# Kernel tuning notes

Measured on AMD Instinct MI355X. Metric: run time of the kernel, lower is better.

The kernel has to match this reference:

```python
import jax, jax.numpy as jnp
import numpy as np

EPS = 1e-8  # torch F.cosine_similarity denominator clamp
NEG = -1e9

def setup_inputs() -> dict:
    key = jax.random.key(0)
    k1, k2, k3 = jax.random.split(key, 3)
    B, H, L, D = 16, 16, 4096, 128
    query = jax.random.normal(k1, (B, H, 1, D), dtype=jnp.float32)
    key_t = jax.random.normal(k2, (B, H, L, D), dtype=jnp.float32)
    mask = jax.random.randint(k3, (B, L), 0, 2, dtype=jnp.int32)
    return {"query": query, "key": key_t, "mask": mask}

def reference(query, key, mask):
    # cosine similarity without materializing the repeated query:
    # scores[b,h,l] = <q[b,h,0],k[b,h,l]> / max(||q||*||k||, eps)
    dots = jnp.einsum('bhod,bhld->bhl', query, key)  # o == 1, [B,H,L]
    qn = jnp.linalg.norm(query, axis=3)              # [B,H,1]
    kn = jnp.linalg.norm(key, axis=3)                # [B,H,L]
    scores = dots / jnp.maximum(qn * kn, EPS)        # [B,H,L]
    m = mask[:, None, :]                              # [B,1,L] broadcast over H
    scores = jnp.where(m == 0, NEG, scores)
    p_attn = jax.nn.softmax(scores, axis=2)
    return p_attn
```

## Files before the change

kernel.cpp:

```cpp
#include <hip/hip_runtime.h>
#include <hip/hip_bf16.h>


constexpr int Bdim = 16, Hdim = 16, Ldim = 4096, Ddim = 128;
constexpr int NTHREADS = 1024;
constexpr float EPSF = 1e-8f;
constexpr float NEGF = -1000000000.0f;

__device__ __forceinline__ float dpp_sum32(float v) {
    v += __int_as_float(__builtin_amdgcn_update_dpp(0, __float_as_int(v), 0x111, 0xf, 0xf, true));
    v += __int_as_float(__builtin_amdgcn_update_dpp(0, __float_as_int(v), 0x112, 0xf, 0xf, true));
    v += __int_as_float(__builtin_amdgcn_update_dpp(0, __float_as_int(v), 0x114, 0xf, 0xf, true));
    v += __int_as_float(__builtin_amdgcn_update_dpp(0, __float_as_int(v), 0x118, 0xf, 0xf, true));
    v += __int_as_float(__builtin_amdgcn_update_dpp(0, __float_as_int(v), 0x142, 0xa, 0xf, true));
    return v;
}

__global__ __launch_bounds__(NTHREADS, 1) void attn_cos_softmax(
    const float* __restrict__ q,
    const float* __restrict__ k,
    const int* __restrict__ mask,
    float* __restrict__ out)
{
    const int bh = blockIdx.x;
    const int b  = bh >> 4;
    const float4* qrow = reinterpret_cast<const float4*>(q + (size_t)bh * Ddim);
    const float4* krow = reinterpret_cast<const float4*>(k + (size_t)bh * Ldim * Ddim);
    const int*    mrow = mask + (size_t)b * Ldim;
    float*        orow = out  + (size_t)bh * Ldim;

    __shared__ float s_scores[Ldim];
    __shared__ float s_redmax[16];
    __shared__ float s_redsum[16];

    const int tid  = threadIdx.x;
    const int g    = tid >> 5;
    const int lane = tid & 31;
    const bool writer = (lane == 31);

    float4 qv = qrow[lane];
    float q2 = qv.x*qv.x + qv.y*qv.y + qv.z*qv.z + qv.w*qv.w;
    q2 = dpp_sum32(q2);
    const float qn = sqrtf(q2);

    constexpr int UNROLL = 16;
    constexpr int ROWS_PER_ITER = 32 * UNROLL;
    #pragma unroll 1
    for (int iter = 0; iter < Ldim / ROWS_PER_ITER; ++iter) {
        const int base = iter * ROWS_PER_ITER + g;
        float4 kv[UNROLL];
        #pragma unroll
        for (int j = 0; j < UNROLL; ++j) {
            kv[j] = krow[(base + j * 32) * (Ddim / 4) + lane];
        }
        #pragma unroll
        for (int j = 0; j < UNROLL; ++j) {
            float dp = kv[j].x*qv.x + kv[j].y*qv.y + kv[j].z*qv.z + kv[j].w*qv.w;
            float k2 = kv[j].x*kv[j].x + kv[j].y*kv[j].y + kv[j].z*kv[j].z + kv[j].w*kv[j].w;
            dp = dpp_sum32(dp);
            k2 = dpp_sum32(k2);
            if (writer) {
                float denom = fmaxf(qn * sqrtf(k2), EPSF);
                s_scores[base + j * 32] = dp / denom;
            }
        }
    }
    __syncthreads();

    float sv[4];
    float lmax = -3.0e9f;
    #pragma unroll
    for (int i = 0; i < 4; ++i) {
        const int idx = tid + i * NTHREADS;
        float s = s_scores[idx];
        s = (mrow[idx] == 0) ? NEGF : s;
        sv[i] = s;
        lmax = fmaxf(lmax, s);
    }
    #pragma unroll
    for (int m = 32; m >= 1; m >>= 1) lmax = fmaxf(lmax, __shfl_xor(lmax, m));
    if ((tid & 63) == 0) s_redmax[tid >> 6] = lmax;
    __syncthreads();
    float gmax = s_redmax[0];
    #pragma unroll
    for (int i = 1; i < 16; ++i) gmax = fmaxf(gmax, s_redmax[i]);

    float ev[4];
    float lsum = 0.0f;
    #pragma unroll
    for (int i = 0; i < 4; ++i) {
        ev[i] = __expf(sv[i] - gmax);
        lsum += ev[i];
    }
    #pragma unroll
    for (int m = 32; m >= 1; m >>= 1) lsum += __shfl_xor(lsum, m);
    if ((tid & 63) == 0) s_redsum[tid >> 6] = lsum;
    __syncthreads();
    float gsum = 0.0f;
    #pragma unroll
    for (int i = 0; i < 16; ++i) gsum += s_redsum[i];
    const float rinv = 1.0f / gsum;

    #pragma unroll
    for (int i = 0; i < 4; ++i) {
        orow[tid + i * NTHREADS] = ev[i] * rinv;
    }
}

extern "C" void kernel_launch(void* const* d_in, const int* in_sizes, int n_in,
                              void* d_out, int out_size, void* d_ws, size_t ws_size,
                              hipStream_t stream) {
    const float* q    = (const float*)d_in[0];
    const float* k    = (const float*)d_in[1];
    const int*   mask = (const int*)d_in[2];
    float*       out  = (float*)d_out;

    dim3 grid(Bdim * Hdim);
    dim3 block(NTHREADS);
    attn_cos_softmax<<<grid, block, 0, stream>>>(q, k, mask, out);
}
```

Before: 104.4 us.

## Split into chunked score kernel and separate vectorized softmax kernel

Splits the fused per-(b,h) kernel into two launches. The first computes cosine scores with 8 chunks per head and 256-thread blocks, raising occupancy to better hide the latency of streaming the keys. The second applies the mask and softmax with float4/int4 vector loads. Scores now round-trip through global memory in the output buffer, and the second launch adds its own overhead.

```diff
diff --git a/kernel.cpp b/kernel.cpp
--- a/kernel.cpp
+++ b/kernel.cpp
@@ -3,7 +3,6 @@
 
 
 constexpr int Bdim = 16, Hdim = 16, Ldim = 4096, Ddim = 128;
-constexpr int NTHREADS = 1024;
 constexpr float EPSF = 1e-8f;
 constexpr float NEGF = -1000000000.0f;
 
@@ -16,22 +15,26 @@
     return v;
 }
 
-__global__ __launch_bounds__(NTHREADS, 1) void attn_cos_softmax(
+constexpr int K1_THREADS = 256;
+constexpr int K1_CHUNKS  = 8;
+constexpr int K1_ROWS    = Ldim / K1_CHUNKS;
+constexpr int K1_UNROLL  = 4;
+constexpr int K1_GROUPS  = K1_THREADS / 32;
+constexpr int K1_RPI     = K1_GROUPS * K1_UNROLL;
+
+__global__ __launch_bounds__(K1_THREADS, 8) void attn_scores(
     const float* __restrict__ q,
     const float* __restrict__ k,
-    const int* __restrict__ mask,
-    float* __restrict__ out)
+    float* __restrict__ scores)
 {
-    const int bh = blockIdx.x;
-    const int b  = bh >> 4;
-    const float4* qrow = reinterpret_cast<const float4*>(q + (size_t)bh * Ddim);
-    const float4* krow = reinterpret_cast<const float4*>(k + (size_t)bh * Ldim * Ddim);
-    const int*    mrow = mask + (size_t)b * Ldim;
-    float*        orow = out  + (size_t)bh * Ldim;
+    const int bid   = blockIdx.x;
+    const int bh    = bid >> 3;
+    const int chunk = bid & (K1_CHUNKS - 1);
+    const int rowbase = chunk * K1_ROWS;
 
-    __shared__ float s_scores[Ldim];
-    __shared__ float s_redmax[16];
-    __shared__ float s_redsum[16];
+    const float4* qrow  = reinterpret_cast<const float4*>(q + (size_t)bh * Ddim);
+    const float4* krow  = reinterpret_cast<const float4*>(k + (size_t)bh * Ldim * Ddim);
+    float*        srow  = scores + (size_t)bh * Ldim;
 
     const int tid  = threadIdx.x;
     const int g    = tid >> 5;
@@ -43,67 +46,84 @@
     q2 = dpp_sum32(q2);
     const float qn = sqrtf(q2);
 
-    constexpr int UNROLL = 16;
-    constexpr int ROWS_PER_ITER = 32 * UNROLL;
     #pragma unroll 1
-    for (int iter = 0; iter < Ldim / ROWS_PER_ITER; ++iter) {
-        const int base = iter * ROWS_PER_ITER + g;
-        float4 kv[UNROLL];
+    for (int iter = 0; iter < K1_ROWS / K1_RPI; ++iter) {
+        const int r0 = rowbase + iter * K1_RPI + g;
+        float4 kv[K1_UNROLL];
         #pragma unroll
-        for (int j = 0; j < UNROLL; ++j) {
-            kv[j] = krow[(base + j * 32) * (Ddim / 4) + lane];
+        for (int j = 0; j < K1_UNROLL; ++j) {
+            kv[j] = krow[(size_t)(r0 + j * K1_GROUPS) * (Ddim / 4) + lane];
         }
         #pragma unroll
-        for (int j = 0; j < UNROLL; ++j) {
+        for (int j = 0; j < K1_UNROLL; ++j) {
             float dp = kv[j].x*qv.x + kv[j].y*qv.y + kv[j].z*qv.z + kv[j].w*qv.w;
             float k2 = kv[j].x*kv[j].x + kv[j].y*kv[j].y + kv[j].z*kv[j].z + kv[j].w*kv[j].w;
             dp = dpp_sum32(dp);
             k2 = dpp_sum32(k2);
             if (writer) {
                 float denom = fmaxf(qn * sqrtf(k2), EPSF);
-                s_scores[base + j * 32] = dp / denom;
+                srow[r0 + j * K1_GROUPS] = dp / denom;
             }
         }
     }
-    __syncthreads();
+}
 
-    float sv[4];
+constexpr int K2_THREADS = 256;
+
+__global__ __launch_bounds__(K2_THREADS) void attn_softmax(
+    float* __restrict__ io,
+    const int* __restrict__ mask)
+{
+    const int bh = blockIdx.x;
+    const int b  = bh >> 4;
+    float4*       srow = reinterpret_cast<float4*>(io + (size_t)bh * Ldim);
+    const int4*   mrow = reinterpret_cast<const int4*>(mask + (size_t)b * Ldim);
+
+    const int tid = threadIdx.x;
+    __shared__ float s_red[4];
+
+    float4 sv[4];
     float lmax = -3.0e9f;
     #pragma unroll
     for (int i = 0; i < 4; ++i) {
-        const int idx = tid + i * NTHREADS;
-        float s = s_scores[idx];
-        s = (mrow[idx] == 0) ? NEGF : s;
+        const int idx = tid + i * K2_THREADS;
+        float4 s = srow[idx];
+        int4   m = mrow[idx];
+        s.x = (m.x == 0) ? NEGF : s.x;
+        s.y = (m.y == 0) ? NEGF : s.y;
+        s.z = (m.z == 0) ? NEGF : s.z;
+        s.w = (m.w == 0) ? NEGF : s.w;
         sv[i] = s;
-        lmax = fmaxf(lmax, s);
+        lmax = fmaxf(lmax, fmaxf(fmaxf(s.x, s.y), fmaxf(s.z, s.w)));
     }
     #pragma unroll
     for (int m = 32; m >= 1; m >>= 1) lmax = fmaxf(lmax, __shfl_xor(lmax, m));
-    if ((tid & 63) == 0) s_redmax[tid >> 6] = lmax;
+    if ((tid & 63) == 0) s_red[tid >> 6] = lmax;
     __syncthreads();
-    float gmax = s_redmax[0];
-    #pragma unroll
-    for (int i = 1; i < 16; ++i) gmax = fmaxf(gmax, s_redmax[i]);
+    const float gmax = fmaxf(fmaxf(s_red[0], s_red[1]), fmaxf(s_red[2], s_red[3]));
+    __syncthreads();
 
-    float ev[4];
     float lsum = 0.0f;
     #pragma unroll
     for (int i = 0; i < 4; ++i) {
-        ev[i] = __expf(sv[i] - gmax);
-        lsum += ev[i];
+        sv[i].x = __expf(sv[i].x - gmax);
+        sv[i].y = __expf(sv[i].y - gmax);
+        sv[i].z = __expf(sv[i].z - gmax);
+        sv[i].w = __expf(sv[i].w - gmax);
+        lsum += (sv[i].x + sv[i].y) + (sv[i].z + sv[i].w);
     }
     #pragma unroll
     for (int m = 32; m >= 1; m >>= 1) lsum += __shfl_xor(lsum, m);
-    if ((tid & 63) == 0) s_redsum[tid >> 6] = lsum;
+    if ((tid & 63) == 0) s_red[tid >> 6] = lsum;
     __syncthreads();
-    float gsum = 0.0f;
-    #pragma unroll
-    for (int i = 0; i < 16; ++i) gsum += s_redsum[i];
+    const float gsum = (s_red[0] + s_red[1]) + (s_red[2] + s_red[3]);
     const float rinv = 1.0f / gsum;
 
     #pragma unroll
     for (int i = 0; i < 4; ++i) {
-        orow[tid + i * NTHREADS] = ev[i] * rinv;
+        float4 s = sv[i];
+        s.x *= rinv; s.y *= rinv; s.z *= rinv; s.w *= rinv;
+        srow[tid + i * K2_THREADS] = s;
     }
 }
 
@@ -115,7 +135,6 @@
     const int*   mask = (const int*)d_in[2];
     float*       out  = (float*)d_out;
 
-    dim3 grid(Bdim * Hdim);
-    dim3 block(NTHREADS);
-    attn_cos_softmax<<<grid, block, 0, stream>>>(q, k, mask, out);
+    attn_scores<<<dim3(Bdim * Hdim * K1_CHUNKS), dim3(K1_THREADS), 0, stream>>>(q, k, out);
+    attn_softmax<<<dim3(Bdim * Hdim), dim3(K2_THREADS), 0, stream>>>(out, mask);
 }
```

New measurement: 109.6 us. 5.0% more time.
